# Kernel tuning notes

Hardware: AMD Instinct MI355X
Metric: run time of the kernel (lower is better)

Reference implementation:

```python
import jax, jax.numpy as jnp
import numpy as np
import math

W = 256      # attention_window
DIL = 1      # attention_dilation
H = 12       # num heads
HD = 64      # head dim
E = 768      # hidden size


def setup_inputs() -> dict:
    key = jax.random.key(0)
    ks = jax.random.split(key, 4)
    B, S = 2, 4096
    s = 0.02
    inp = {"hidden_states": jax.random.normal(ks[0], (B, S, E), jnp.float32)}
    inp["Wq"] = jax.random.normal(ks[1], (E, E), jnp.float32) * s
    inp["Wk"] = jax.random.normal(ks[2], (E, E), jnp.float32) * s
    inp["Wv"] = jax.random.normal(ks[3], (E, E), jnp.float32) * s
    inp["bq"] = jnp.zeros((E,), jnp.float32)
    inp["bk"] = jnp.zeros((E,), jnp.float32)
    inp["bv"] = jnp.zeros((E,), jnp.float32)
    return inp


def _banded_attention(q, k, v):
    # q,k,v: [B,S,H,HD]; banded attention with window W, dilation DIL
    B, S, Hh, D = q.shape
    offsets = (jnp.arange(2 * W + 1) - W) * DIL  # relative key offsets
    pos = jnp.arange(S)

    def score(off):
        idx = pos + off
        valid = (idx >= 0) & (idx < S)          # mask_invalid_locations
        kk = k[:, jnp.clip(idx, 0, S - 1)]      # [B,S,H,HD] shifted keys
        s = jnp.einsum('bshd,bshd->bsh', q, kk)
        return jnp.where(valid[None, :, None], s, -jnp.inf)

    # diagonaled_mm(q, k): [2W+1, B, S, H] -> [B, S, H, 2W+1]
    scores = jax.lax.map(score, offsets)
    probs = jax.nn.softmax(jnp.moveaxis(scores, 0, -1), axis=-1)

    # diagonaled_mm(probs, v, is_t1_diagonaled=True): accumulate over band
    def step(acc, j):
        off = offsets[j]
        idx = pos + off
        valid = (idx >= 0) & (idx < S)
        vv = v[:, jnp.clip(idx, 0, S - 1)]
        p = jnp.where(valid[None, :, None], probs[..., j], 0.0)
        return acc + p[..., None] * vv, None

    out, _ = jax.lax.scan(step, jnp.zeros_like(v), jnp.arange(2 * W + 1))
    return out


def reference(hidden_states, Wq, bq, Wk, bk, Wv, bv):
    B, S, _ = hidden_states.shape
    q = (hidden_states @ Wq.T + bq) / math.sqrt(HD)
    k = hidden_states @ Wk.T + bk
    v = hidden_states @ Wv.T + bv
    q = q.reshape(B, S, H, HD)
    k = k.reshape(B, S, H, HD)
    v = v.reshape(B, S, H, HD)
    out = _banded_attention(q, k, v)  # [B,S,H,HD]
    return out.reshape(B, S, E)
```

## Files before the change

### kernel.cpp

```cpp
#include <hip/hip_runtime.h>

#define S_LEN 4096
#define BATCH 2
#define EMB   768
#define NH    12
#define HDIM  64
#define WIN   256

using f32x4  = __attribute__((ext_vector_type(4))) float;
using bf16x8 = __attribute__((ext_vector_type(8))) short;
using u16x4  = __attribute__((ext_vector_type(4))) unsigned short;
using u16x8  = __attribute__((ext_vector_type(8))) unsigned short;

#define AS1 __attribute__((address_space(1)))
#define AS3 __attribute__((address_space(3)))

__device__ __forceinline__ unsigned short f2bf(float x) {
    unsigned int u = __float_as_uint(x);
    return (unsigned short)((u + 0x7fffu + ((u >> 16) & 1u)) >> 16);
}

__global__ void cvt_kernel(const float* __restrict__ in,
                           unsigned short* __restrict__ out, int n8) {
    int i = blockIdx.x * blockDim.x + threadIdx.x;
    if (i >= n8) return;
    const float4* p = reinterpret_cast<const float4*>(in) + (size_t)i * 2;
    float4 a = p[0];
    float4 b = p[1];
    u16x8 o;
    o[0] = f2bf(a.x); o[1] = f2bf(a.y); o[2] = f2bf(a.z); o[3] = f2bf(a.w);
    o[4] = f2bf(b.x); o[5] = f2bf(b.y); o[6] = f2bf(b.z); o[7] = f2bf(b.w);
    reinterpret_cast<u16x8*>(out)[i] = o;
}

__global__ void cvt3_kernel(const float* __restrict__ w0, const float* __restrict__ w1,
                            const float* __restrict__ w2,
                            unsigned short* __restrict__ o0, unsigned short* __restrict__ o1,
                            unsigned short* __restrict__ o2, int n8) {
    int i = blockIdx.x * blockDim.x + threadIdx.x;
    if (i >= n8) return;
    const float* in = (blockIdx.y == 0) ? w0 : (blockIdx.y == 1) ? w1 : w2;
    unsigned short* out = (blockIdx.y == 0) ? o0 : (blockIdx.y == 1) ? o1 : o2;
    const float4* p = reinterpret_cast<const float4*>(in) + (size_t)i * 2;
    float4 a = p[0];
    float4 b = p[1];
    u16x8 o;
    o[0] = f2bf(a.x); o[1] = f2bf(a.y); o[2] = f2bf(a.z); o[3] = f2bf(a.w);
    o[4] = f2bf(b.x); o[5] = f2bf(b.y); o[6] = f2bf(b.z); o[7] = f2bf(b.w);
    reinterpret_cast<u16x8*>(out)[i] = o;
}

#define NKT (EMB / 32)

__global__ __launch_bounds__(256) void qkv_gemm(
    const unsigned short* __restrict__ A,
    const unsigned short* __restrict__ Wq,
    const unsigned short* __restrict__ Wk,
    const unsigned short* __restrict__ Wv,
    const float* __restrict__ bq,
    const float* __restrict__ bk,
    const float* __restrict__ bv,
    unsigned short* __restrict__ qo,
    unsigned short* __restrict__ ko,
    unsigned short* __restrict__ vo)
{
    __shared__ unsigned short As[2][128 * 32];
    __shared__ unsigned short Bs[2][128 * 32];

    const int tid  = threadIdx.x;
    const int lane = tid & 63;
    const int wave = tid >> 6;

    const int mblk = blockIdx.x;
    const int nblk = blockIdx.y;
    const int wsel = nblk / 6;
    const int nloc0 = (nblk % 6) * 128;
    const unsigned short* Wp = (wsel == 0) ? Wq : ((wsel == 1) ? Wk : Wv);
    const int wm = wave >> 1, wn = wave & 1;

    f32x4 acc[4][4];
#pragma unroll
    for (int i = 0; i < 4; ++i)
#pragma unroll
        for (int j = 0; j < 4; ++j)
            acc[i][j] = (f32x4){0.f, 0.f, 0.f, 0.f};

    const int frow = lane & 15;
    const int g    = lane >> 4;

    const char* Abase = (const char*)(A  + (size_t)(mblk * 128) * EMB);
    const char* Bbase = (const char*)(Wp + (size_t)nloc0 * EMB);

    const int srow = tid >> 2;
    const int pb   = tid & 3;
    const int sblk = pb ^ ((srow >> 1) & 3);

#define GLDS(gp, lp) __builtin_amdgcn_global_load_lds((const AS1 unsigned int*)(gp), (AS3 unsigned int*)(lp), 16, 0, 0)
#define STG(q, t) do {                                                                                   \
    GLDS(Abase + (size_t)srow * 1536 + (t) * 64 + sblk * 16,        &As[q][srow * 32 + pb * 8]);         \
    GLDS(Abase + (size_t)(64 + srow) * 1536 + (t) * 64 + sblk * 16, &As[q][(64 + srow) * 32 + pb * 8]);  \
    GLDS(Bbase + (size_t)srow * 1536 + (t) * 64 + sblk * 16,        &Bs[q][srow * 32 + pb * 8]);         \
    GLDS(Bbase + (size_t)(64 + srow) * 1536 + (t) * 64 + sblk * 16, &Bs[q][(64 + srow) * 32 + pb * 8]);  \
} while (0)

    auto rdA = [&](int q, int mi) -> bf16x8 {
        int r = wm * 64 + mi * 16 + frow;
        return *reinterpret_cast<const bf16x8*>(&As[q][r * 32 + (g ^ ((r >> 1) & 3)) * 8]);
    };
    auto rdB = [&](int q, int ni) -> bf16x8 {
        int r = wn * 64 + ni * 16 + frow;
        return *reinterpret_cast<const bf16x8*>(&Bs[q][r * 32 + (g ^ ((r >> 1) & 3)) * 8]);
    };

#define KLOOP(SW) do {                                                                        \
    STG(0, 0);                                                                                \
    asm volatile("s_waitcnt vmcnt(0)" ::: "memory");                                          \
    __syncthreads();                                                                          \
    int cur = 0;                                                                              \
    _Pragma("unroll 1")                                                                       \
    for (int t = 0; t < NKT; ++t) {                                                           \
        if (t + 1 < NKT) STG(cur ^ 1, t + 1);                                                 \
        bf16x8 afr[4], bfr[4];                                                                \
        _Pragma("unroll") for (int ni = 0; ni < 4; ++ni) bfr[ni] = rdB(cur, ni);              \
        _Pragma("unroll") for (int mi = 0; mi < 4; ++mi) afr[mi] = rdA(cur, mi);              \
        __builtin_amdgcn_s_setprio(1);                                                        \
        _Pragma("unroll") for (int mi = 0; mi < 4; ++mi)                                      \
            _Pragma("unroll") for (int ni = 0; ni < 4; ++ni)                                  \
                acc[mi][ni] = (SW)                                                            \
                    ? __builtin_amdgcn_mfma_f32_16x16x32_bf16(bfr[ni], afr[mi], acc[mi][ni], 0, 0, 0)  \
                    : __builtin_amdgcn_mfma_f32_16x16x32_bf16(afr[mi], bfr[ni], acc[mi][ni], 0, 0, 0); \
        __builtin_amdgcn_s_setprio(0);                                                        \
        if (t + 1 < NKT) {                                                                    \
            asm volatile("s_waitcnt vmcnt(0)" ::: "memory");                                  \
            __syncthreads();                                                                  \
            cur ^= 1;                                                                         \
        }                                                                                     \
    }                                                                                         \
} while (0)

    if (wsel < 2) {
        KLOOP(1);
        const float* bias = (wsel == 0) ? bq : bk;
        unsigned short* op = (wsel == 0) ? qo : ko;
        const float qs = (wsel == 0) ? 0.125f : 1.0f;
#pragma unroll
        for (int mi = 0; mi < 4; ++mi) {
            int m = mblk * 128 + wm * 64 + mi * 16 + frow;
            int b = m >> 12, s = m & 4095;
#pragma unroll
            for (int ni = 0; ni < 4; ++ni) {
                int n0 = nloc0 + wn * 64 + ni * 16 + g * 4;
                float4 bb = *reinterpret_cast<const float4*>(&bias[n0]);
                int h = n0 >> 6, hd0 = n0 & 63;
                u16x4 pk;
                pk[0] = f2bf((acc[mi][ni][0] + bb.x) * qs);
                pk[1] = f2bf((acc[mi][ni][1] + bb.y) * qs);
                pk[2] = f2bf((acc[mi][ni][2] + bb.z) * qs);
                pk[3] = f2bf((acc[mi][ni][3] + bb.w) * qs);
                *reinterpret_cast<u16x4*>(&op[((size_t)(b * NH + h) * S_LEN + s) * HDIM + hd0]) = pk;
            }
        }
    } else {
        KLOOP(0);
#pragma unroll
        for (int mi = 0; mi < 4; ++mi) {
            int m0 = mblk * 128 + wm * 64 + mi * 16 + g * 4;
            int b = m0 >> 12, s0 = m0 & 4095;
#pragma unroll
            for (int ni = 0; ni < 4; ++ni) {
                int n = nloc0 + wn * 64 + ni * 16 + frow;
                float bb = bv[n];
                int h = n >> 6, hd = n & 63;
                u16x4 pk;
                pk[0] = f2bf(acc[mi][ni][0] + bb);
                pk[1] = f2bf(acc[mi][ni][1] + bb);
                pk[2] = f2bf(acc[mi][ni][2] + bb);
                pk[3] = f2bf(acc[mi][ni][3] + bb);
                *reinterpret_cast<u16x4*>(&vo[((size_t)(b * NH + h) * HDIM + hd) * S_LEN + s0]) = pk;
            }
        }
    }
}

#define QB   128
#define KC   64
#define NCHQ ((QB + 2 * WIN) / KC)

#define STAGE_ATT(buf, ks) do {                                                              \
    const unsigned short* kr_ = kp + (size_t)((ks) + srow) * HDIM + gblk * 8;                \
    __builtin_amdgcn_global_load_lds(                                                        \
        (const AS1 unsigned int*)kr_,                                                        \
        (AS3 unsigned int*)&Ksm[buf][wave * 512], 16, 0, 0);                                 \
    const unsigned short* vr_ = vp + (size_t)srow * S_LEN + (ks) + gblk * 8;                 \
    __builtin_amdgcn_global_load_lds(                                                        \
        (const AS1 unsigned int*)vr_,                                                        \
        (AS3 unsigned int*)&Vsm[buf][wave * 512], 16, 0, 0);                                 \
} while (0)

__global__ __launch_bounds__(512) void banded_attn(
    const unsigned short* __restrict__ qg,
    const unsigned short* __restrict__ kg,
    const unsigned short* __restrict__ vtg,
    float* __restrict__ out)
{
    __shared__ unsigned short Ksm[2][KC * HDIM];
    __shared__ unsigned short Vsm[2][HDIM * KC];
    __shared__ unsigned short Psm[8][16 * KC];

    const int tid  = threadIdx.x;
    const int wave = tid >> 6, lane = tid & 63;
    const int qb = blockIdx.x * QB;
    const int h  = blockIdx.y, b = blockIdx.z;

    const unsigned short* qp = qg  + (size_t)(b * NH + h) * S_LEN * HDIM;
    const unsigned short* kp = kg  + (size_t)(b * NH + h) * S_LEN * HDIM;
    const unsigned short* vp = vtg + (size_t)(b * NH + h) * HDIM * S_LEN;

    const int frow = lane & 15;
    const int g    = lane >> 4;
    const int fcol = g * 8;

    const int srow = tid >> 3;
    const int gblk = (tid & 7) ^ (srow & 7);

    bf16x8 qf[2];
    {
        const unsigned short* qr = qp + (size_t)(qb + wave * 16 + frow) * HDIM;
        qf[0] = *reinterpret_cast<const bf16x8*>(qr + fcol);
        qf[1] = *reinterpret_cast<const bf16x8*>(qr + 32 + fcol);
    }

    float l_part[4];
    f32x4 o_acc[4];
#pragma unroll
    for (int r = 0; r < 4; ++r) l_part[r] = 0.f;
#pragma unroll
    for (int ni = 0; ni < 4; ++ni) o_acc[ni] = (f32x4){0.f, 0.f, 0.f, 0.f};

    const int c_start = (qb < WIN) ? ((WIN - qb) >> 6) : 0;
    const int c_end   = min(NCHQ, (S_LEN + WIN - qb) >> 6);
    const int qrow0 = qb + wave * 16 + g * 4;

    const int w_lo = qb + wave * 16 - WIN;
    const int w_hi = qb + wave * 16 + 15 + WIN;

    STAGE_ATT(0, qb - WIN + c_start * KC);
    asm volatile("s_waitcnt vmcnt(0)" ::: "memory");
    __syncthreads();

    int cur = 0;
    for (int c = c_start; c < c_end; ++c) {
        const int ks = qb - WIN + c * KC;
        if (c + 1 < c_end) STAGE_ATT(cur ^ 1, ks + KC);

        const bool active = (ks + KC - 1 >= w_lo) && (ks <= w_hi);
        if (active) {
            f32x4 sc[4];
#pragma unroll
            for (int ni = 0; ni < 4; ++ni) sc[ni] = (f32x4){0.f, 0.f, 0.f, 0.f};
#pragma unroll
            for (int ni = 0; ni < 4; ++ni) {
                int krow = ni * 16 + frow;
                int sw   = (krow & 7) << 3;
                bf16x8 kf0 = *reinterpret_cast<const bf16x8*>(&Ksm[cur][krow * KC + (fcol ^ sw)]);
                bf16x8 kf1 = *reinterpret_cast<const bf16x8*>(&Ksm[cur][krow * KC + ((32 + fcol) ^ sw)]);
                sc[ni] = __builtin_amdgcn_mfma_f32_16x16x32_bf16(qf[0], kf0, sc[ni], 0, 0, 0);
                sc[ni] = __builtin_amdgcn_mfma_f32_16x16x32_bf16(qf[1], kf1, sc[ni], 0, 0, 0);
            }

            float pm[4][4];
#pragma unroll
            for (int ni = 0; ni < 4; ++ni) {
                int d0 = qrow0 - (ks + ni * 16 + frow);
#pragma unroll
                for (int r = 0; r < 4; ++r) {
                    bool valid = (unsigned)(d0 + r + WIN) <= (unsigned)(2 * WIN);
                    pm[ni][r] = valid ? __expf(sc[ni][r]) : 0.f;
                }
            }
#pragma unroll
            for (int r = 0; r < 4; ++r) {
                l_part[r] += (pm[0][r] + pm[1][r]) + (pm[2][r] + pm[3][r]);
                int prow = g * 4 + r;
#pragma unroll
                for (int ni = 0; ni < 4; ++ni) {
                    int pelem = (ni * 16 + frow) ^ ((prow & 7) << 3);
                    Psm[wave][prow * KC + pelem] = f2bf(pm[ni][r]);
                }
            }

            asm volatile("s_waitcnt lgkmcnt(0)" ::: "memory");
            __builtin_amdgcn_sched_barrier(0);

            bf16x8 pf[2];
#pragma unroll
            for (int kk = 0; kk < 2; ++kk) {
                int sw = (frow & 7) << 3;
                pf[kk] = *reinterpret_cast<const bf16x8*>(&Psm[wave][frow * KC + ((kk * 32 + fcol) ^ sw)]);
            }
#pragma unroll
            for (int ni = 0; ni < 4; ++ni) {
                int vrow = ni * 16 + frow;
                int sw   = (vrow & 7) << 3;
#pragma unroll
                for (int kk = 0; kk < 2; ++kk) {
                    bf16x8 vf = *reinterpret_cast<const bf16x8*>(&Vsm[cur][vrow * KC + ((kk * 32 + fcol) ^ sw)]);
                    o_acc[ni] = __builtin_amdgcn_mfma_f32_16x16x32_bf16(pf[kk], vf, o_acc[ni], 0, 0, 0);
                }
            }
        }

        asm volatile("s_waitcnt vmcnt(0)" ::: "memory");
        __syncthreads();
        cur ^= 1;
    }

#pragma unroll
    for (int d = 1; d < 16; d <<= 1)
#pragma unroll
        for (int r = 0; r < 4; ++r)
            l_part[r] += __shfl_xor(l_part[r], d, 64);

#pragma unroll
    for (int r = 0; r < 4; ++r) {
        float inv = 1.0f / l_part[r];
        int s = qrow0 + r;
        size_t obase = ((size_t)b * S_LEN + s) * EMB + h * HDIM;
#pragma unroll
        for (int ni = 0; ni < 4; ++ni)
            out[obase + ni * 16 + frow] = o_acc[ni][r] * inv;
    }
}

extern "C" void kernel_launch(void* const* d_in, const int* in_sizes, int n_in,
                              void* d_out, int out_size, void* d_ws, size_t ws_size,
                              hipStream_t stream) {
    const float* hs = (const float*)d_in[0];
    const float* Wq = (const float*)d_in[1];
    const float* Wk = (const float*)d_in[2];
    const float* Wv = (const float*)d_in[3];
    const float* bq = (const float*)d_in[4];
    const float* bk = (const float*)d_in[5];
    const float* bv = (const float*)d_in[6];
    float* out = (float*)d_out;

    char* w = (char*)d_ws;
    unsigned short* hs_bf = (unsigned short*)w;
    unsigned short* wq_bf = (unsigned short*)(w + 12582912);
    unsigned short* wk_bf = wq_bf + 589824;
    unsigned short* wv_bf = wk_bf + 589824;
    unsigned short* q_ws  = (unsigned short*)(w + 12582912 + 3 * 1179648);
    unsigned short* k_ws  = q_ws + 6291456;
    unsigned short* v_ws  = k_ws + 6291456;

    cvt_kernel<<<3072, 256, 0, stream>>>(hs, hs_bf, 786432);
    cvt3_kernel<<<dim3(288, 3), 256, 0, stream>>>(Wq, Wk, Wv, wq_bf, wk_bf, wv_bf, 73728);

    qkv_gemm<<<dim3(64, 18), 256, 0, stream>>>(hs_bf, wq_bf, wk_bf, wv_bf,
                                               bq, bk, bv, q_ws, k_ws, v_ws);

    banded_attn<<<dim3(S_LEN / QB, NH, BATCH), 512, 0, stream>>>(q_ws, k_ws, v_ws, out);
}
```

Baseline: 97.20 us.

## Merge conversion launches, skip band masking on interior chunks, cheapen bf16 rounding

```diff
diff --git a/kernel.cpp b/kernel.cpp
--- a/kernel.cpp
+++ b/kernel.cpp
@@ -19,28 +19,27 @@
     unsigned int u = __float_as_uint(x);
     return (unsigned short)((u + 0x7fffu + ((u >> 16) & 1u)) >> 16);
 }
-
-__global__ void cvt_kernel(const float* __restrict__ in,
-                           unsigned short* __restrict__ out, int n8) {
-    int i = blockIdx.x * blockDim.x + threadIdx.x;
-    if (i >= n8) return;
-    const float4* p = reinterpret_cast<const float4*>(in) + (size_t)i * 2;
-    float4 a = p[0];
-    float4 b = p[1];
-    u16x8 o;
-    o[0] = f2bf(a.x); o[1] = f2bf(a.y); o[2] = f2bf(a.z); o[3] = f2bf(a.w);
-    o[4] = f2bf(b.x); o[5] = f2bf(b.y); o[6] = f2bf(b.z); o[7] = f2bf(b.w);
-    reinterpret_cast<u16x8*>(out)[i] = o;
-}
-
-__global__ void cvt3_kernel(const float* __restrict__ w0, const float* __restrict__ w1,
-                            const float* __restrict__ w2,
-                            unsigned short* __restrict__ o0, unsigned short* __restrict__ o1,
-                            unsigned short* __restrict__ o2, int n8) {
-    int i = blockIdx.x * blockDim.x + threadIdx.x;
-    if (i >= n8) return;
-    const float* in = (blockIdx.y == 0) ? w0 : (blockIdx.y == 1) ? w1 : w2;
-    unsigned short* out = (blockIdx.y == 0) ? o0 : (blockIdx.y == 1) ? o1 : o2;
+__device__ __forceinline__ unsigned short f2bf_fast(float x) {
+    return (unsigned short)((__float_as_uint(x) + 0x8000u) >> 16);
+}
+
+__global__ void cvt_all_kernel(const float* __restrict__ hs, const float* __restrict__ w0,
+                               const float* __restrict__ w1, const float* __restrict__ w2,
+                               unsigned short* __restrict__ ohs, unsigned short* __restrict__ o0,
+                               unsigned short* __restrict__ o1, unsigned short* __restrict__ o2) {
+    int blk = blockIdx.x;
+    const float* in;
+    unsigned short* out;
+    int i;
+    if (blk < 3072) { in = hs; out = ohs; i = blk * 256 + threadIdx.x; if (i >= 786432) return; }
+    else {
+        int wsel = (blk - 3072) / 288;
+        int wblk = (blk - 3072) % 288;
+        in  = (wsel == 0) ? w0 : (wsel == 1) ? w1 : w2;
+        out = (wsel == 0) ? o0 : (wsel == 1) ? o1 : o2;
+        i = wblk * 256 + threadIdx.x;
+        if (i >= 73728) return;
+    }
     const float4* p = reinterpret_cast<const float4*>(in) + (size_t)i * 2;
     float4 a = p[0];
     float4 b = p[1];
@@ -239,10 +238,23 @@
 
     const int c_start = (qb < WIN) ? ((WIN - qb) >> 6) : 0;
     const int c_end   = min(NCHQ, (S_LEN + WIN - qb) >> 6);
-    const int qrow0 = qb + wave * 16 + g * 4;
-
-    const int w_lo = qb + wave * 16 - WIN;
-    const int w_hi = qb + wave * 16 + 15 + WIN;
+    const int qw    = qb + wave * 16;
+    const int qrow0 = qw + g * 4;
+
+    const int w_lo = qw - WIN;
+    const int w_hi = qw + 15 + WIN;
+
+    int kb[4];
+#pragma unroll
+    for (int ni = 0; ni < 4; ++ni) kb[ni] = ni * 16 + frow;
+    unsigned short* prow_p[4];
+    int swz_r[4];
+#pragma unroll
+    for (int r = 0; r < 4; ++r) {
+        int prow = g * 4 + r;
+        prow_p[r] = &Psm[wave][prow * KC];
+        swz_r[r]  = (prow & 7) << 3;
+    }
 
     STAGE_ATT(0, qb - WIN + c_start * KC);
     asm volatile("s_waitcnt vmcnt(0)" ::: "memory");
@@ -268,25 +280,31 @@
                 sc[ni] = __builtin_amdgcn_mfma_f32_16x16x32_bf16(qf[1], kf1, sc[ni], 0, 0, 0);
             }
 
+            const bool full = (ks >= qw - 241) && (ks <= qw + 193);
             float pm[4][4];
-#pragma unroll
-            for (int ni = 0; ni < 4; ++ni) {
-                int d0 = qrow0 - (ks + ni * 16 + frow);
-#pragma unroll
-                for (int r = 0; r < 4; ++r) {
-                    bool valid = (unsigned)(d0 + r + WIN) <= (unsigned)(2 * WIN);
-                    pm[ni][r] = valid ? __expf(sc[ni][r]) : 0.f;
+            if (full) {
+#pragma unroll
+                for (int ni = 0; ni < 4; ++ni)
+#pragma unroll
+                    for (int r = 0; r < 4; ++r)
+                        pm[ni][r] = __expf(sc[ni][r]);
+            } else {
+#pragma unroll
+                for (int ni = 0; ni < 4; ++ni) {
+                    int d0 = qrow0 - (ks + kb[ni]);
+#pragma unroll
+                    for (int r = 0; r < 4; ++r) {
+                        bool valid = (unsigned)(d0 + r + WIN) <= (unsigned)(2 * WIN);
+                        pm[ni][r] = valid ? __expf(sc[ni][r]) : 0.f;
+                    }
                 }
             }
 #pragma unroll
             for (int r = 0; r < 4; ++r) {
                 l_part[r] += (pm[0][r] + pm[1][r]) + (pm[2][r] + pm[3][r]);
-                int prow = g * 4 + r;
-#pragma unroll
-                for (int ni = 0; ni < 4; ++ni) {
-                    int pelem = (ni * 16 + frow) ^ ((prow & 7) << 3);
-                    Psm[wave][prow * KC + pelem] = f2bf(pm[ni][r]);
-                }
+#pragma unroll
+                for (int ni = 0; ni < 4; ++ni)
+                    prow_p[r][kb[ni] ^ swz_r[r]] = f2bf_fast(pm[ni][r]);
             }
 
             asm volatile("s_waitcnt lgkmcnt(0)" ::: "memory");
@@ -353,8 +371,7 @@
     unsigned short* k_ws  = q_ws + 6291456;
     unsigned short* v_ws  = k_ws + 6291456;
 
-    cvt_kernel<<<3072, 256, 0, stream>>>(hs, hs_bf, 786432);
-    cvt3_kernel<<<dim3(288, 3), 256, 0, stream>>>(Wq, Wk, Wv, wq_bf, wk_bf, wv_bf, 73728);
+    cvt_all_kernel<<<3936, 256, 0, stream>>>(hs, Wq, Wk, Wv, hs_bf, wq_bf, wk_bf, wv_bf);
 
     qkv_gemm<<<dim3(64, 18), 256, 0, stream>>>(hs_bf, wq_bf, wk_bf, wv_bf,
                                                bq, bk, bv, q_ws, k_ws, v_ws);
```

Result: faster. 93.83 us (-3.5%).
